# Performance work log

Hardware: AMD Instinct MI355X
Metric: run time of the kernel (lower is better)

## Reference

```python
import jax, jax.numpy as jnp
import numpy as np

N_NODES = 100000
N_EDGES = 1600000


def _norms(src, dst, n_nodes, dtype):
    # DGL GraphConv norm='both': scale src by out-degree^{-1/2}, dst by in-degree^{-1/2}
    ones = jnp.ones((src.shape[0],), dtype=dtype)
    deg_out = jax.ops.segment_sum(ones, src, num_segments=n_nodes)
    deg_in = jax.ops.segment_sum(ones, dst, num_segments=n_nodes)
    inv_sqrt_out = jnp.where(deg_out > 0, jax.lax.rsqrt(jnp.maximum(deg_out, 1.0)), 0.0)
    inv_sqrt_in = jnp.where(deg_in > 0, jax.lax.rsqrt(jnp.maximum(deg_in, 1.0)), 0.0)
    return inv_sqrt_out, inv_sqrt_in


def _graph_conv(x, W, src, dst, inv_sqrt_out, inv_sqrt_in, n_nodes, relu):
    # norm='both': out = D_in^{-1/2} A D_out^{-1/2} x W
    h = x * inv_sqrt_out[:, None]
    h = h @ W                      # dense transform before aggregation
    msg = h[src]                   # gather messages along edges [E, F]
    agg = jax.ops.segment_sum(msg, dst, num_segments=n_nodes)
    out = agg * inv_sqrt_in[:, None]
    return jax.nn.relu(out) if relu else out


def setup_inputs() -> dict:
    key = jax.random.key(0)
    k1, k2, k3, k4, k5, k6 = jax.random.split(key, 6)
    in_dim, h_dim, out_dim = 128, 128, 64
    features = jax.random.normal(k1, (N_NODES, in_dim), dtype=jnp.float32)
    W1 = jax.random.normal(k2, (in_dim, h_dim), dtype=jnp.float32) * (1.0 / np.sqrt(in_dim))
    W2 = jax.random.normal(k3, (h_dim, h_dim), dtype=jnp.float32) * (1.0 / np.sqrt(h_dim))
    W3 = jax.random.normal(k4, (h_dim, out_dim), dtype=jnp.float32) * (1.0 / np.sqrt(h_dim))
    src = jax.random.randint(k5, (N_EDGES,), 0, N_NODES, dtype=jnp.int32)
    dst = jax.random.randint(k6, (N_EDGES,), 0, N_NODES, dtype=jnp.int32)
    return {"features": features, "W1": W1, "W2": W2, "W3": W3, "src": src, "dst": dst}


def reference(features, W1, W2, W3, src, dst):
    inv_sqrt_out, inv_sqrt_in = _norms(src, dst, N_NODES, features.dtype)
    h = _graph_conv(features, W1, src, dst, inv_sqrt_out, inv_sqrt_in, N_NODES, relu=True)
    h = _graph_conv(h, W2, src, dst, inv_sqrt_out, inv_sqrt_in, N_NODES, relu=True)
    h = _graph_conv(h, W3, src, dst, inv_sqrt_out, inv_sqrt_in, N_NODES, relu=False)
    return h
```

## Files before the change

kernel.cpp:

```cpp
#include <hip/hip_runtime.h>


typedef float f32x4 __attribute__((ext_vector_type(4)));
typedef __bf16 bf16x8 __attribute__((ext_vector_type(8)));

constexpr int CAP = 5120;
constexpr int MAXNB = 400;

__device__ inline unsigned short f2bf_bits(float f) {
    unsigned u = __float_as_uint(f);
    unsigned r = u + 0x7fff + ((u >> 16) & 1);
    return (unsigned short)(r >> 16);
}
__device__ inline float bf_bits2f(unsigned short s) {
    return __uint_as_float(((unsigned)s) << 16);
}
__device__ inline float bf_lo(unsigned v) { return __uint_as_float(v << 16); }
__device__ inline float bf_hi(unsigned v) { return __uint_as_float(v & 0xffff0000u); }


__global__ __launch_bounds__(512) void bucket_scatter(
    const int* __restrict__ src, const int* __restrict__ dst,
    int* __restrict__ cur_d, int* __restrict__ cur_s,
    int* __restrict__ bpair, int* __restrict__ bsrc, int E, int NB) {
    __shared__ int hd[MAXNB], hs[MAXNB], bd[MAXNB], bs[MAXNB];
    const int tid = threadIdx.x;
    for (int i = tid; i < NB; i += 512) { hd[i] = 0; hs[i] = 0; }
    __syncthreads();

    const int base = (blockIdx.x * 512 + tid) * 8;
    int s[8], d[8], rd[8], rs[8];
    bool va[8];
    if (base + 8 <= E) {
        const int4 s0 = *(const int4*)(src + base);
        const int4 s1 = *(const int4*)(src + base + 4);
        const int4 d0 = *(const int4*)(dst + base);
        const int4 d1 = *(const int4*)(dst + base + 4);
        s[0] = s0.x; s[1] = s0.y; s[2] = s0.z; s[3] = s0.w;
        s[4] = s1.x; s[5] = s1.y; s[6] = s1.z; s[7] = s1.w;
        d[0] = d0.x; d[1] = d0.y; d[2] = d0.z; d[3] = d0.w;
        d[4] = d1.x; d[5] = d1.y; d[6] = d1.z; d[7] = d1.w;
#pragma unroll
        for (int j = 0; j < 8; ++j) va[j] = true;
    } else {
#pragma unroll
        for (int j = 0; j < 8; ++j) {
            const int e = base + j;
            va[j] = e < E;
            const int ec = va[j] ? e : 0;
            s[j] = src[ec];
            d[j] = dst[ec];
        }
    }
#pragma unroll
    for (int j = 0; j < 8; ++j) {
        if (va[j]) {
            rd[j] = atomicAdd(&hd[d[j] >> 8], 1);
            rs[j] = atomicAdd(&hs[s[j] >> 8], 1);
        }
    }
    __syncthreads();
    for (int i = tid; i < NB; i += 512) {
        bd[i] = hd[i] ? atomicAdd(&cur_d[i], hd[i]) : 0;
        bs[i] = hs[i] ? atomicAdd(&cur_s[i], hs[i]) : 0;
    }
    __syncthreads();
#pragma unroll
    for (int j = 0; j < 8; ++j) {
        if (va[j]) {
            const int b = d[j] >> 8;
            const int pos = bd[b] + rd[j];
            if (pos < CAP) bpair[(size_t)b * CAP + pos] = (s[j] << 8) | (d[j] & 255);
            const int c = s[j] >> 8;
            const int ps = bs[c] + rs[j];
            if (ps < CAP) bsrc[(size_t)c * CAP + ps] = s[j];
        }
    }
}

__global__ __launch_bounds__(512) void bucket_scan(
    const int* __restrict__ cur_d, int* __restrict__ bbase, int NB) {
    __shared__ int s[512];
    const int tid = threadIdx.x;
    s[tid] = (tid < NB) ? cur_d[tid] : 0;
    __syncthreads();
    for (int off = 1; off < 512; off <<= 1) {
        int v = (tid >= off) ? s[tid - off] : 0;
        __syncthreads();
        s[tid] += v;
        __syncthreads();
    }
    if (tid < NB) bbase[tid] = (tid > 0) ? s[tid - 1] : 0;
}

__global__ __launch_bounds__(256) void csr_outdeg(
    const int* __restrict__ bpair, const int* __restrict__ bsrc,
    const int* __restrict__ bcnt_d, const int* __restrict__ bcnt_s,
    const int* __restrict__ bbase, int* __restrict__ row_ptr,
    int* __restrict__ col, float* __restrict__ isi, float* __restrict__ iso,
    float* __restrict__ fscale, int N, int NB) {
    __shared__ int h[256], hs[256], sc[256], cur[256];
    const int b = blockIdx.x;
    const int tid = threadIdx.x;
    const int cnt = min(bcnt_d[b], CAP);
    const int scnt = min(bcnt_s[b], CAP);
    const int base = bbase[b];
    const int* pairs = bpair + (size_t)b * CAP;
    const int* svals = bsrc + (size_t)b * CAP;
    h[tid] = 0;
    hs[tid] = 0;
    __syncthreads();
    for (int i = tid; i < cnt; i += 256) atomicAdd(&h[pairs[i] & 255], 1);
    for (int i = tid; i < scnt; i += 256) atomicAdd(&hs[svals[i] & 255], 1);
    __syncthreads();
    sc[tid] = h[tid];
    __syncthreads();
    for (int off = 1; off < 256; off <<= 1) {
        int v = (tid >= off) ? sc[tid - off] : 0;
        __syncthreads();
        sc[tid] += v;
        __syncthreads();
    }
    const int lp = sc[tid] - h[tid];
    const int node = b * 256 + tid;
    if (node < N) {
        row_ptr[node] = base + lp;
        const float di = (h[tid] > 0) ? rsqrtf((float)h[tid]) : 0.f;
        const float dw = (hs[tid] > 0) ? rsqrtf((float)hs[tid]) : 0.f;
        isi[node] = di;
        iso[node] = dw;
        fscale[node] = di * dw;
    }
    if (b == NB - 1 && tid == 0) row_ptr[N] = base + cnt;
    cur[tid] = lp;
    __syncthreads();
    for (int i = tid; i < cnt; i += 256) {
        const int p = pairs[i];
        const int pos = base + atomicAdd(&cur[p & 255], 1);
        col[pos] = p >> 8;
    }
}


__device__ inline void wpack1(const float* W, unsigned short* Wh,
                              unsigned short* Wl, int t, int F) {
    const int n = t >> 7, k = t & 127;
    const float w = W[k * F + n];
    const unsigned short hb = f2bf_bits(w);
    Wh[t] = hb;
    Wl[t] = f2bf_bits(w - bf_bits2f(hb));
}

__global__ __launch_bounds__(256) void wpack_all(
    const float* __restrict__ W1, const float* __restrict__ W2,
    const float* __restrict__ W3, unsigned short* __restrict__ Wt1h,
    unsigned short* __restrict__ Wt1l, unsigned short* __restrict__ Wt2h,
    unsigned short* __restrict__ Wt2l, unsigned short* __restrict__ Wt3h,
    unsigned short* __restrict__ Wt3l) {
    int t = blockIdx.x * 256 + threadIdx.x;
    if (t < 16384) {
        wpack1(W1, Wt1h, Wt1l, t, 128);
    } else if (t < 32768) {
        wpack1(W2, Wt2h, Wt2l, t - 16384, 128);
    } else if (t < 40960) {
        wpack1(W3, Wt3h, Wt3l, t - 32768, 64);
    }
}


template <int F>
__global__ __launch_bounds__(256) void gemm_mfma(
    const float* __restrict__ X, const unsigned short* __restrict__ Wt_hi,
    const unsigned short* __restrict__ Wt_lo, const float* __restrict__ so,
    unsigned short* __restrict__ Y, int N) {
    constexpr int NT = F / 16;
    const int wave = threadIdx.x >> 6;
    const int lane = threadIdx.x & 63;
    const int r0 = blockIdx.x * 128 + wave * 32;
    const int l15 = lane & 15;
    const int quad = lane >> 4;

    const int rowA0 = min(r0 + l15, N - 1);
    const int rowA1 = min(r0 + 16 + l15, N - 1);
    const float s0 = so[rowA0];
    const float s1 = so[rowA1];
    const float* pX0 = X + (size_t)rowA0 * 128 + quad * 8;
    const float* pX1 = X + (size_t)rowA1 * 128 + quad * 8;

    f32x4 acc0[NT], acc1[NT];
    const f32x4 z = {0.f, 0.f, 0.f, 0.f};
#pragma unroll
    for (int t = 0; t < NT; ++t) { acc0[t] = z; acc1[t] = z; }

    union AB { bf16x8 v; unsigned short u[8]; };

#pragma unroll
    for (int s = 0; s < 4; ++s) {
        const int kb = s * 32;
        AB bh[NT], bl[NT];
#pragma unroll
        for (int t = 0; t < NT; ++t) {
            const int n = t * 16 + l15;
            bh[t].v = *(const bf16x8*)(Wt_hi + n * 128 + kb + quad * 8);
            bl[t].v = *(const bf16x8*)(Wt_lo + n * 128 + kb + quad * 8);
        }
        float a[8];
        *(f32x4*)&a[0] = *(const f32x4*)(pX0 + kb);
        *(f32x4*)&a[4] = *(const f32x4*)(pX0 + kb + 4);
        AB ah, al;
#pragma unroll
        for (int j = 0; j < 8; ++j) {
            float x = a[j] * s0;
            unsigned short hb = f2bf_bits(x);
            ah.u[j] = hb;
            al.u[j] = f2bf_bits(x - bf_bits2f(hb));
        }
#pragma unroll
        for (int t = 0; t < NT; ++t) {
            acc0[t] = __builtin_amdgcn_mfma_f32_16x16x32_bf16(ah.v, bh[t].v, acc0[t], 0, 0, 0);
            acc0[t] = __builtin_amdgcn_mfma_f32_16x16x32_bf16(al.v, bh[t].v, acc0[t], 0, 0, 0);
            acc0[t] = __builtin_amdgcn_mfma_f32_16x16x32_bf16(ah.v, bl[t].v, acc0[t], 0, 0, 0);
        }
        *(f32x4*)&a[0] = *(const f32x4*)(pX1 + kb);
        *(f32x4*)&a[4] = *(const f32x4*)(pX1 + kb + 4);
#pragma unroll
        for (int j = 0; j < 8; ++j) {
            float x = a[j] * s1;
            unsigned short hb = f2bf_bits(x);
            ah.u[j] = hb;
            al.u[j] = f2bf_bits(x - bf_bits2f(hb));
        }
#pragma unroll
        for (int t = 0; t < NT; ++t) {
            acc1[t] = __builtin_amdgcn_mfma_f32_16x16x32_bf16(ah.v, bh[t].v, acc1[t], 0, 0, 0);
            acc1[t] = __builtin_amdgcn_mfma_f32_16x16x32_bf16(al.v, bh[t].v, acc1[t], 0, 0, 0);
            acc1[t] = __builtin_amdgcn_mfma_f32_16x16x32_bf16(ah.v, bl[t].v, acc1[t], 0, 0, 0);
        }
    }

#pragma unroll
    for (int t = 0; t < NT; ++t) {
#pragma unroll
        for (int r = 0; r < 4; ++r) {
            int node0 = r0 + quad * 4 + r;
            if (node0 < N) Y[(size_t)node0 * F + t * 16 + l15] = f2bf_bits(acc0[t][r]);
            int node1 = r0 + 16 + quad * 4 + r;
            if (node1 < N) Y[(size_t)node1 * F + t * 16 + l15] = f2bf_bits(acc1[t][r]);
        }
    }
}


template <int F>
__global__ __launch_bounds__(256) void fused_gather_gemm(
    const unsigned short* __restrict__ msg, const int* __restrict__ row_ptr,
    const int* __restrict__ col, const float* __restrict__ fscale,
    const unsigned short* __restrict__ Wt_hi, const unsigned short* __restrict__ Wt_lo,
    unsigned short* __restrict__ Yout, int N) {
    __shared__ __align__(16) unsigned Asw[32 * 64];
    constexpr int CT = F / 64;
    const int wave = threadIdx.x >> 6;
    const int lane = threadIdx.x & 63;
    const int d0 = blockIdx.x * 32;
    const int l15 = lane & 15;
    const int quad = lane >> 4;
    const int cbase = wave * (F / 4);
    const unsigned* m32 = (const unsigned*)msg;

    bf16x8 wh[4][CT], wl[4][CT];
#pragma unroll
    for (int s = 0; s < 4; ++s)
#pragma unroll
        for (int bt = 0; bt < CT; ++bt) {
            const int n = cbase + bt * 16 + l15;
            wh[s][bt] = *(const bf16x8*)(Wt_hi + n * 128 + s * 32 + quad * 8);
            wl[s][bt] = *(const bf16x8*)(Wt_lo + n * 128 + s * 32 + quad * 8);
        }

#pragma unroll 1
    for (int i = 0; i < 8; ++i) {
        const int r = wave * 8 + i;
        const int d = d0 + r;
        float a0 = 0.f, a1 = 0.f, b0 = 0.f, b1 = 0.f;
        if (d < N) {
            const int start = row_ptr[d], end = row_ptr[d + 1];
            int e = start;
            const int efull = start + ((end - start) & ~7);
            for (; e < efull; e += 8) {
                int c[8];
#pragma unroll
                for (int j = 0; j < 8; ++j) c[j] = col[e + j];
                unsigned v[8];
#pragma unroll
                for (int j = 0; j < 8; ++j)
                    v[j] = m32[(unsigned)c[j] * 64u + (unsigned)lane];
#pragma unroll
                for (int j = 0; j < 8; j += 2) {
                    a0 += bf_lo(v[j]);     a1 += bf_hi(v[j]);
                    b0 += bf_lo(v[j + 1]); b1 += bf_hi(v[j + 1]);
                }
            }
            const int rem = end - e;
            if (rem > 0) {
                int c[8];
#pragma unroll
                for (int j = 0; j < 8; ++j) c[j] = col[e + min(j, rem - 1)];
                unsigned v[8];
#pragma unroll
                for (int j = 0; j < 8; ++j)
                    v[j] = m32[(unsigned)c[j] * 64u + (unsigned)lane];
#pragma unroll
                for (int j = 0; j < 8; ++j) {
                    a0 += (j < rem) ? bf_lo(v[j]) : 0.f;
                    a1 += (j < rem) ? bf_hi(v[j]) : 0.f;
                }
            }
            const float sc = fscale[d];
            a0 = fmaxf((a0 + b0) * sc, 0.f);
            a1 = fmaxf((a1 + b1) * sc, 0.f);
        }
        const unsigned packed =
            ((unsigned)f2bf_bits(a1) << 16) | (unsigned)f2bf_bits(a0);
        Asw[r * 64 + (lane ^ ((r & 7) << 2))] = packed;
    }
    __syncthreads();

    f32x4 acc[2][CT];
    const f32x4 z = {0.f, 0.f, 0.f, 0.f};
#pragma unroll
    for (int rt = 0; rt < 2; ++rt)
#pragma unroll
        for (int bt = 0; bt < CT; ++bt) acc[rt][bt] = z;

#pragma unroll
    for (int s = 0; s < 4; ++s) {
        bf16x8 a[2];
#pragma unroll
        for (int rt = 0; rt < 2; ++rt) {
            const int row = rt * 16 + l15;
            const int dw = (s * 16 + quad * 4) ^ ((row & 7) << 2);
            a[rt] = *(const bf16x8*)&Asw[row * 64 + dw];
        }
#pragma unroll
        for (int rt = 0; rt < 2; ++rt)
#pragma unroll
            for (int bt = 0; bt < CT; ++bt) {
                acc[rt][bt] = __builtin_amdgcn_mfma_f32_16x16x32_bf16(a[rt], wh[s][bt], acc[rt][bt], 0, 0, 0);
                acc[rt][bt] = __builtin_amdgcn_mfma_f32_16x16x32_bf16(a[rt], wl[s][bt], acc[rt][bt], 0, 0, 0);
            }
    }

#pragma unroll
    for (int rt = 0; rt < 2; ++rt)
#pragma unroll
        for (int bt = 0; bt < CT; ++bt) {
#pragma unroll
            for (int r = 0; r < 4; ++r) {
                const int node = d0 + rt * 16 + quad * 4 + r;
                if (node < N)
                    Yout[(size_t)node * F + cbase + bt * 16 + l15] =
                        f2bf_bits(acc[rt][bt][r]);
            }
        }
}


__global__ __launch_bounds__(256) void gather64(
    const unsigned short* __restrict__ msg, const int* __restrict__ row_ptr,
    const int* __restrict__ col, const float* __restrict__ isi,
    float* __restrict__ out, int N) {
    const int w = (blockIdx.x * 256 + threadIdx.x) >> 6;
    const int lane = threadIdx.x & 63;
    const int node = w * 2 + (lane >> 5);
    const int j31 = lane & 31;
    if (node >= N) return;
    const int start = row_ptr[node], end = row_ptr[node + 1];
    const unsigned* m32 = (const unsigned*)msg;

    float a0 = 0.f, a1 = 0.f, b0 = 0.f, b1 = 0.f;
    int e = start;
    const int efull = start + ((end - start) & ~7);
    for (; e < efull; e += 8) {
        int c[8];
#pragma unroll
        for (int j = 0; j < 8; ++j) c[j] = col[e + j];
        unsigned v[8];
#pragma unroll
        for (int j = 0; j < 8; ++j)
            v[j] = m32[(unsigned)c[j] * 32u + (unsigned)j31];
#pragma unroll
        for (int j = 0; j < 8; j += 2) {
            a0 += bf_lo(v[j]);     a1 += bf_hi(v[j]);
            b0 += bf_lo(v[j + 1]); b1 += bf_hi(v[j + 1]);
        }
    }
    const int rem = end - e;
    if (rem > 0) {
        int c[8];
#pragma unroll
        for (int j = 0; j < 8; ++j) c[j] = col[e + min(j, rem - 1)];
        unsigned v[8];
#pragma unroll
        for (int j = 0; j < 8; ++j)
            v[j] = m32[(unsigned)c[j] * 32u + (unsigned)j31];
#pragma unroll
        for (int j = 0; j < 8; ++j) {
            a0 += (j < rem) ? bf_lo(v[j]) : 0.f;
            a1 += (j < rem) ? bf_hi(v[j]) : 0.f;
        }
    }
    const float sc = isi[node];
    *(float2*)(out + (size_t)node * 64 + j31 * 2) =
        make_float2((a0 + b0) * sc, (a1 + b1) * sc);
}


extern "C" void kernel_launch(void* const* d_in, const int* in_sizes, int n_in,
                              void* d_out, int out_size, void* d_ws, size_t ws_size,
                              hipStream_t stream) {
    const float* features = (const float*)d_in[0];
    const float* W1 = (const float*)d_in[1];
    const float* W2 = (const float*)d_in[2];
    const float* W3 = (const float*)d_in[3];
    const int* src = (const int*)d_in[4];
    const int* dst = (const int*)d_in[5];
    float* out = (float*)d_out;

    const int N = in_sizes[0] / 128;
    const int E = in_sizes[4];
    const int NB = (N + 255) >> 8;

    char* ws = (char*)d_ws;
    unsigned short* A = (unsigned short*)ws;      ws += (size_t)N * 128 * 2;
    unsigned short* Y = (unsigned short*)ws;      ws += (size_t)N * 128 * 2;
    int* row_ptr = (int*)ws;                      ws += (size_t)(N + 1) * 4;
    int* col = (int*)ws;                          ws += (size_t)E * 4;
    float* iso = (float*)ws;                      ws += (size_t)N * 4;
    float* isi = (float*)ws;                      ws += (size_t)N * 4;
    float* fscale = (float*)ws;                   ws += (size_t)N * 4;
    int* cur_d = (int*)ws;                        ws += MAXNB * 4;
    int* cur_s = (int*)ws;                        ws += MAXNB * 4;
    int* bbase = (int*)ws;                        ws += MAXNB * 4;
    unsigned short* Wt1h = (unsigned short*)ws;   ws += 128 * 128 * 2;
    unsigned short* Wt1l = (unsigned short*)ws;   ws += 128 * 128 * 2;
    unsigned short* Wt2h = (unsigned short*)ws;   ws += 128 * 128 * 2;
    unsigned short* Wt2l = (unsigned short*)ws;   ws += 128 * 128 * 2;
    unsigned short* Wt3h = (unsigned short*)ws;   ws += 64 * 128 * 2;
    unsigned short* Wt3l = (unsigned short*)ws;   ws += 64 * 128 * 2;

    int* bpair = (int*)A;
    int* bsrc = (int*)((char*)A + (size_t)MAXNB * CAP * 4);

    wpack_all<<<160, 256, 0, stream>>>(W1, W2, W3, Wt1h, Wt1l, Wt2h, Wt2l, Wt3h, Wt3l);
    hipMemsetAsync(cur_d, 0, 2 * MAXNB * sizeof(int), stream);
    const int gBS = (E + 4095) / 4096;
    bucket_scatter<<<gBS, 512, 0, stream>>>(src, dst, cur_d, cur_s, bpair, bsrc, E, NB);
    bucket_scan<<<1, 512, 0, stream>>>(cur_d, bbase, NB);
    csr_outdeg<<<NB, 256, 0, stream>>>(bpair, bsrc, cur_d, cur_s, bbase, row_ptr,
                                       col, isi, iso, fscale, N, NB);

    const int gG = (N + 127) / 128;
    const int gF = (N + 31) / 32;
    const int ga64 = ((N / 2 + 1) * 64 + 255) / 256;

    gemm_mfma<128><<<gG, 256, 0, stream>>>(features, Wt1h, Wt1l, iso, Y, N);
    fused_gather_gemm<128><<<gF, 256, 0, stream>>>(Y, row_ptr, col, fscale,
                                                   Wt2h, Wt2l, A, N);
    fused_gather_gemm<64><<<gF, 256, 0, stream>>>(A, row_ptr, col, fscale,
                                                  Wt3h, Wt3l, Y, N);
    gather64<<<ga64, 256, 0, stream>>>(Y, row_ptr, col, isi, out, N);
}
```

Before: 435.5 us.

## Fold bucket scan and memset into neighboring kernels, defer weight loads

Removes the separate single-block bucket_scan launch: each csr_outdeg block now computes its own prefix base by reducing the preceding bucket counts in shared memory. The hipMemsetAsync that cleared the bucket cursors is folded into wpack_all. In fused_gather_gemm, the weight fragments are loaded per k-step right before the MFMAs instead of being held in registers across the gather loop. This reduces register pressure during the gather and should raise occupancy, at the cost of re-reading weights from cache. The net effect is two fewer launches, traded for redundant per-block reduction work.

```diff
diff --git a/kernel.cpp b/kernel.cpp
--- a/kernel.cpp
+++ b/kernel.cpp
@@ -78,33 +78,29 @@
     }
 }
 
-__global__ __launch_bounds__(512) void bucket_scan(
-    const int* __restrict__ cur_d, int* __restrict__ bbase, int NB) {
-    __shared__ int s[512];
-    const int tid = threadIdx.x;
-    s[tid] = (tid < NB) ? cur_d[tid] : 0;
-    __syncthreads();
-    for (int off = 1; off < 512; off <<= 1) {
-        int v = (tid >= off) ? s[tid - off] : 0;
-        __syncthreads();
-        s[tid] += v;
-        __syncthreads();
-    }
-    if (tid < NB) bbase[tid] = (tid > 0) ? s[tid - 1] : 0;
-}
-
 __global__ __launch_bounds__(256) void csr_outdeg(
     const int* __restrict__ bpair, const int* __restrict__ bsrc,
     const int* __restrict__ bcnt_d, const int* __restrict__ bcnt_s,
-    const int* __restrict__ bbase, int* __restrict__ row_ptr,
-    int* __restrict__ col, float* __restrict__ isi, float* __restrict__ iso,
+    int* __restrict__ row_ptr, int* __restrict__ col,
+    float* __restrict__ isi, float* __restrict__ iso,
     float* __restrict__ fscale, int N, int NB) {
-    __shared__ int h[256], hs[256], sc[256], cur[256];
+    __shared__ int h[256], hs[256], sc[256], cur[256], red[256];
     const int b = blockIdx.x;
     const int tid = threadIdx.x;
     const int cnt = min(bcnt_d[b], CAP);
     const int scnt = min(bcnt_s[b], CAP);
-    const int base = bbase[b];
+
+    int partial = 0;
+    for (int i = tid; i < b; i += 256) partial += bcnt_d[i];
+    red[tid] = partial;
+    __syncthreads();
+#pragma unroll
+    for (int off = 128; off > 0; off >>= 1) {
+        if (tid < off) red[tid] += red[tid + off];
+        __syncthreads();
+    }
+    const int base = red[0];
+
     const int* pairs = bpair + (size_t)b * CAP;
     const int* svals = bsrc + (size_t)b * CAP;
     h[tid] = 0;
@@ -156,8 +152,9 @@
     const float* __restrict__ W3, unsigned short* __restrict__ Wt1h,
     unsigned short* __restrict__ Wt1l, unsigned short* __restrict__ Wt2h,
     unsigned short* __restrict__ Wt2l, unsigned short* __restrict__ Wt3h,
-    unsigned short* __restrict__ Wt3l) {
+    unsigned short* __restrict__ Wt3l, int* __restrict__ cur_zero) {
     int t = blockIdx.x * 256 + threadIdx.x;
+    if (t < 2 * MAXNB) cur_zero[t] = 0;
     if (t < 16384) {
         wpack1(W1, Wt1h, Wt1l, t, 128);
     } else if (t < 32768) {
@@ -258,24 +255,10 @@
     const unsigned short* __restrict__ Wt_hi, const unsigned short* __restrict__ Wt_lo,
     unsigned short* __restrict__ Yout, int N) {
     __shared__ __align__(16) unsigned Asw[32 * 64];
-    constexpr int CT = F / 64;
     const int wave = threadIdx.x >> 6;
     const int lane = threadIdx.x & 63;
     const int d0 = blockIdx.x * 32;
-    const int l15 = lane & 15;
-    const int quad = lane >> 4;
-    const int cbase = wave * (F / 4);
     const unsigned* m32 = (const unsigned*)msg;
-
-    bf16x8 wh[4][CT], wl[4][CT];
-#pragma unroll
-    for (int s = 0; s < 4; ++s)
-#pragma unroll
-        for (int bt = 0; bt < CT; ++bt) {
-            const int n = cbase + bt * 16 + l15;
-            wh[s][bt] = *(const bf16x8*)(Wt_hi + n * 128 + s * 32 + quad * 8);
-            wl[s][bt] = *(const bf16x8*)(Wt_lo + n * 128 + s * 32 + quad * 8);
-        }
 
 #pragma unroll 1
     for (int i = 0; i < 8; ++i) {
@@ -325,6 +308,11 @@
     }
     __syncthreads();
 
+    constexpr int CT = F / 64;
+    const int l15 = lane & 15;
+    const int quad = lane >> 4;
+    const int cbase = wave * (F / 4);
+
     f32x4 acc[2][CT];
     const f32x4 z = {0.f, 0.f, 0.f, 0.f};
 #pragma unroll
@@ -341,12 +329,19 @@
             const int dw = (s * 16 + quad * 4) ^ ((row & 7) << 2);
             a[rt] = *(const bf16x8*)&Asw[row * 64 + dw];
         }
+        bf16x8 bh[CT], bl[CT];
+#pragma unroll
+        for (int bt = 0; bt < CT; ++bt) {
+            const int n = cbase + bt * 16 + l15;
+            bh[bt] = *(const bf16x8*)(Wt_hi + n * 128 + s * 32 + quad * 8);
+            bl[bt] = *(const bf16x8*)(Wt_lo + n * 128 + s * 32 + quad * 8);
+        }
 #pragma unroll
         for (int rt = 0; rt < 2; ++rt)
 #pragma unroll
             for (int bt = 0; bt < CT; ++bt) {
-                acc[rt][bt] = __builtin_amdgcn_mfma_f32_16x16x32_bf16(a[rt], wh[s][bt], acc[rt][bt], 0, 0, 0);
-                acc[rt][bt] = __builtin_amdgcn_mfma_f32_16x16x32_bf16(a[rt], wl[s][bt], acc[rt][bt], 0, 0, 0);
+                acc[rt][bt] = __builtin_amdgcn_mfma_f32_16x16x32_bf16(a[rt], bh[bt], acc[rt][bt], 0, 0, 0);
+                acc[rt][bt] = __builtin_amdgcn_mfma_f32_16x16x32_bf16(a[rt], bl[bt], acc[rt][bt], 0, 0, 0);
             }
     }
 
@@ -440,7 +435,6 @@
     float* fscale = (float*)ws;                   ws += (size_t)N * 4;
     int* cur_d = (int*)ws;                        ws += MAXNB * 4;
     int* cur_s = (int*)ws;                        ws += MAXNB * 4;
-    int* bbase = (int*)ws;                        ws += MAXNB * 4;
     unsigned short* Wt1h = (unsigned short*)ws;   ws += 128 * 128 * 2;
     unsigned short* Wt1l = (unsigned short*)ws;   ws += 128 * 128 * 2;
     unsigned short* Wt2h = (unsigned short*)ws;   ws += 128 * 128 * 2;
@@ -451,12 +445,11 @@
     int* bpair = (int*)A;
     int* bsrc = (int*)((char*)A + (size_t)MAXNB * CAP * 4);
 
-    wpack_all<<<160, 256, 0, stream>>>(W1, W2, W3, Wt1h, Wt1l, Wt2h, Wt2l, Wt3h, Wt3l);
-    hipMemsetAsync(cur_d, 0, 2 * MAXNB * sizeof(int), stream);
+    wpack_all<<<160, 256, 0, stream>>>(W1, W2, W3, Wt1h, Wt1l, Wt2h, Wt2l,
+                                       Wt3h, Wt3l, cur_d);
     const int gBS = (E + 4095) / 4096;
     bucket_scatter<<<gBS, 512, 0, stream>>>(src, dst, cur_d, cur_s, bpair, bsrc, E, NB);
-    bucket_scan<<<1, 512, 0, stream>>>(cur_d, bbase, NB);
-    csr_outdeg<<<NB, 256, 0, stream>>>(bpair, bsrc, cur_d, cur_s, bbase, row_ptr,
+    csr_outdeg<<<NB, 256, 0, stream>>>(bpair, bsrc, cur_d, cur_s, row_ptr,
                                        col, isi, iso, fscale, N, NB);
 
     const int gG = (N + 127) / 128;
```

Measured after the change: 373.4 us. -14.3%, faster.
